# Optimization experiments

Hardware: AMD Instinct MI355X
Metric: run time of the kernel (lower is better)

The kernel has to match this reference:

```python
import jax, jax.numpy as jnp
import numpy as np

NHEAD = 16
EPS = 1e-5


def layer_norm(x, w, b):
    mu = jnp.mean(x, axis=-1, keepdims=True)
    var = jnp.var(x, axis=-1, keepdims=True)
    return (x - mu) * jax.lax.rsqrt(var + EPS) * w + b


def setup_inputs() -> dict:
    key = jax.random.key(0)
    ks = jax.random.split(key, 14)
    B, S, E, F = 16, 1024, 1024, 4096
    s = 0.02
    return {
        "x": jax.random.normal(ks[0], (B, S, E), jnp.float32),
        "in_proj_w": jax.random.normal(ks[1], (3 * E, E), jnp.float32) * s,
        "in_proj_b": jax.random.normal(ks[2], (3 * E,), jnp.float32) * s,
        "out_w": jax.random.normal(ks[3], (E, E), jnp.float32) * s,
        "out_b": jax.random.normal(ks[4], (E,), jnp.float32) * s,
        "lin1_w": jax.random.normal(ks[5], (F, E), jnp.float32) * s,
        "lin1_b": jax.random.normal(ks[6], (F,), jnp.float32) * s,
        "lin2_w": jax.random.normal(ks[7], (E, F), jnp.float32) * s,
        "lin2_b": jax.random.normal(ks[8], (E,), jnp.float32) * s,
        "norm1_w": jnp.ones((E,), jnp.float32),
        "norm1_b": jnp.zeros((E,), jnp.float32),
        "norm2_w": jnp.ones((E,), jnp.float32),
        "norm2_b": jnp.zeros((E,), jnp.float32),
    }


def reference(x, in_proj_w, in_proj_b, out_w, out_b, lin1_w, lin1_b, lin2_w, lin2_b,
              norm1_w, norm1_b, norm2_w, norm2_b):
    B, S, E = x.shape
    H = NHEAD
    D = E // H

    # --- pre-norm self-attention (q = k = v = norm1(x)) ---
    xn = layer_norm(x, norm1_w, norm1_b)
    qkv = xn @ in_proj_w.T + in_proj_b                      # [B,S,3E]
    q, k, v = jnp.split(qkv, 3, axis=-1)
    q = q.reshape(B, S, H, D)
    k = k.reshape(B, S, H, D)
    v = v.reshape(B, S, H, D)
    scale = 1.0 / jnp.sqrt(jnp.asarray(D, x.dtype))
    scores = jnp.einsum("bqhd,bkhd->bhqk", q, k) * scale    # [B,H,S,S]
    attn = jax.nn.softmax(scores, axis=-1)
    ctx = jnp.einsum("bhqk,bkhd->bqhd", attn, v).reshape(B, S, E)
    attn_out = ctx @ out_w.T + out_b
    x = x + attn_out

    # --- pre-norm feedforward (gelu) ---
    xn2 = layer_norm(x, norm2_w, norm2_b)
    h = jax.nn.gelu(xn2 @ lin1_w.T + lin1_b, approximate=False)
    x = x + (h @ lin2_w.T + lin2_b)
    return x
```

## Files before the change

kernel.cpp:

```cpp
#include <hip/hip_runtime.h>


typedef __attribute__((ext_vector_type(8))) short bf16x8;
typedef __attribute__((ext_vector_type(4))) float f32x4;
typedef __attribute__((ext_vector_type(8))) unsigned short u16x8;
typedef __attribute__((ext_vector_type(4))) unsigned short u16x4;

__device__ __forceinline__ float bf2f(unsigned short u) {
    return __uint_as_float(((unsigned int)u) << 16);
}
__device__ __forceinline__ unsigned short f2bf(float f) {
    unsigned int u = __float_as_uint(f);
    u += 0x7fffu + ((u >> 16) & 1u);
    return (unsigned short)(u >> 16);
}
__device__ __forceinline__ unsigned int pkbf_trunc(float a, float b) {
    return (__float_as_uint(a) >> 16) | (__float_as_uint(b) & 0xffff0000u);
}

__device__ __forceinline__ float fast_gelu(float v) {
    const float x = v * 0.70710678118654752f;
    const float ax = fabsf(x);
    const float t = __builtin_amdgcn_rcpf(fmaf(0.3275911f, ax, 1.0f));
    float p = fmaf(1.061405429f, t, -1.453152027f);
    p = fmaf(p, t, 1.421413741f);
    p = fmaf(p, t, -0.284496736f);
    p = fmaf(p, t, 0.254829592f);
    p = p * t;
    const float e = __expf(-x * x);
    float erfv = fmaf(-p, e, 1.0f);
    erfv = (x < 0.0f) ? -erfv : erfv;
    return 0.5f * v * (1.0f + erfv);
}

__device__ __forceinline__ void gload_lds16(const unsigned short* g, unsigned short* l) {
    __builtin_amdgcn_global_load_lds(
        (const __attribute__((address_space(1))) unsigned int*)g,
        (__attribute__((address_space(3))) unsigned int*)l, 16, 0, 0);
}

#define FENCE() asm volatile("" ::: "memory")
#define BAR()                         \
    do {                              \
        FENCE();                      \
        __builtin_amdgcn_s_barrier(); \
        FENCE();                      \
    } while (0)
#define VMCNT(n)                                               \
    do {                                                       \
        asm volatile("s_waitcnt vmcnt(" #n ")" ::: "memory");  \
        __builtin_amdgcn_sched_barrier(0);                     \
    } while (0)

__global__ __launch_bounds__(256) void cvt_kernel(const float* __restrict__ in,
                                                  unsigned short* __restrict__ out, int n4) {
    int i = blockIdx.x * 256 + threadIdx.x;
    if (i >= n4) return;
    float4 v = ((const float4*)in)[i];
    u16x4 o;
    o[0] = f2bf(v.x); o[1] = f2bf(v.y); o[2] = f2bf(v.z); o[3] = f2bf(v.w);
    ((u16x4*)out)[i] = o;
}

__global__ __launch_bounds__(256) void ln_kernel(const float* __restrict__ x,
                                                 const float* __restrict__ w,
                                                 const float* __restrict__ b,
                                                 unsigned short* __restrict__ out) {
    const int row = blockIdx.x;
    const int t = threadIdx.x;
    const float* xr = x + (size_t)row * 1024;
    float4 v = *(const float4*)(xr + t * 4);
    float s = v.x + v.y + v.z + v.w;
    float sq = v.x * v.x + v.y * v.y + v.z * v.z + v.w * v.w;
#pragma unroll
    for (int off = 32; off > 0; off >>= 1) {
        s += __shfl_xor(s, off);
        sq += __shfl_xor(sq, off);
    }
    __shared__ float rs_[4], rq_[4];
    if ((t & 63) == 0) { rs_[t >> 6] = s; rq_[t >> 6] = sq; }
    __syncthreads();
    s = rs_[0] + rs_[1] + rs_[2] + rs_[3];
    sq = rq_[0] + rq_[1] + rq_[2] + rq_[3];
    const float mu = s * (1.0f / 1024.0f);
    const float var = sq * (1.0f / 1024.0f) - mu * mu;
    const float rstd = rsqrtf(var + 1e-5f);
    const int c = t * 4;
    float4 wv = *(const float4*)(w + c);
    float4 bv = *(const float4*)(b + c);
    u16x4 o;
    o[0] = f2bf((v.x - mu) * rstd * wv.x + bv.x);
    o[1] = f2bf((v.y - mu) * rstd * wv.y + bv.y);
    o[2] = f2bf((v.z - mu) * rstd * wv.z + bv.z);
    o[3] = f2bf((v.w - mu) * rstd * wv.w + bv.w);
    *(u16x4*)(out + (size_t)row * 1024 + c) = o;
}

template <int EPI>
__global__ __launch_bounds__(512, 2) void gemm_bt(const unsigned short* __restrict__ A,
                                                  const unsigned short* __restrict__ Bt,
                                                  const float* __restrict__ bias,
                                                  const float* __restrict__ resid,
                                                  void* __restrict__ outp,
                                                  int M, int N, int K, int cnt) {
    __shared__ __align__(16) unsigned short sA[2][256 * 64];
    __shared__ __align__(16) unsigned short sB[2][256 * 64];
    const int t = threadIdx.x;
    const int lane = t & 63;
    const int w = t >> 6;
    const int wm = w >> 2;
    const int wn = w & 3;
    const int quad = lane >> 4;
    const int cl = lane & 15;

    const int GY = M >> 8;
    const int gyl = 31 - __clz(GY);
    const int nt = GY * (N >> 8);
    const int NB = gridDim.x;
    const int g = blockIdx.x;

#define DECODE(gg, mB, nB)                                   \
    do {                                                     \
        const int l_ = ((gg) & 7) * (nt >> 3) + ((gg) >> 3); \
        const int nq_ = l_ >> gyl;                           \
        (nB) = nq_ << 8;                                     \
        (mB) = (l_ - (nq_ << gyl)) << 8;                     \
    } while (0)

    const int swz0 = (quad ^ (cl & 7)) * 16;
    const int swz1 = ((quad + 4) ^ (cl & 7)) * 16;
    const char* aB0 = (const char*)sA + (wm * 128 + cl) * 128 + swz0;
    const char* aB1 = (const char*)sA + (wm * 128 + cl) * 128 + swz1;
    const char* bB0 = (const char*)sB + (wn * 64 + cl) * 128 + swz0;
    const char* bB1 = (const char*)sB + (wn * 64 + cl) * 128 + swz1;

    const int rl = lane >> 3;
    const size_t o8 = (size_t)8 * K;
    const size_t o128 = (size_t)128 * K;
    const size_t thr = (size_t)(w * 16 + rl) * K + (size_t)(((lane & 7) ^ rl) * 8);

#define STG(gp, sbuf, buf, hf, k0)                                                        \
    do {                                                                                  \
        gload_lds16((gp) + (k0) + thr + (hf) * o128,                                      \
                    &sbuf[buf][((hf) * 128 + w * 16) * 64]);                              \
        gload_lds16((gp) + (k0) + thr + (hf) * o128 + o8,                                 \
                    &sbuf[buf][((hf) * 128 + w * 16 + 8) * 64]);                          \
    } while (0)
#define READ_B8(buf)                                                                      \
    do {                                                                                  \
        _Pragma("unroll") for (int nf_ = 0; nf_ < 4; ++nf_) {                             \
            bfr[nf_][0] = *(const bf16x8*)(bB0 + (buf) * 32768 + nf_ * 2048);             \
            bfr[nf_][1] = *(const bf16x8*)(bB1 + (buf) * 32768 + nf_ * 2048);             \
        }                                                                                 \
    } while (0)
#define READ_A2(buf, mfb)                                                                 \
    do {                                                                                  \
        af[0][0] = *(const bf16x8*)(aB0 + (buf) * 32768 + (mfb) * 2048);                  \
        af[0][1] = *(const bf16x8*)(aB1 + (buf) * 32768 + (mfb) * 2048);                  \
        af[1][0] = *(const bf16x8*)(aB0 + (buf) * 32768 + ((mfb) + 1) * 2048);            \
        af[1][1] = *(const bf16x8*)(aB1 + (buf) * 32768 + ((mfb) + 1) * 2048);            \
    } while (0)
#define MFMA_Q(q)                                                                         \
    do {                                                                                  \
        __builtin_amdgcn_s_setprio(1);                                                    \
        _Pragma("unroll") for (int m_ = 0; m_ < 2; ++m_)                                  \
            _Pragma("unroll") for (int nf_ = 0; nf_ < 4; ++nf_)                           \
                _Pragma("unroll") for (int ks_ = 0; ks_ < 2; ++ks_)                       \
                    acc[2 * (q) + m_][nf_] = __builtin_amdgcn_mfma_f32_16x16x32_bf16(     \
                        af[m_][ks_], bfr[nf_][ks_], acc[2 * (q) + m_][nf_], 0, 0, 0);     \
        __builtin_amdgcn_s_setprio(0);                                                    \
    } while (0)

    f32x4 acc[8][4] = {};
    bf16x8 bfr[4][2];
    bf16x8 af[2][2];

    int mBc, nBc, mBn, nBn;
    DECODE(g, mBc, nBc);
    const unsigned short* gAc = A + (size_t)mBc * K;
    const unsigned short* gBc = Bt + (size_t)nBc * K;
    int kc = 0;
    mBn = mBc; nBn = nBc;
    const unsigned short* gAn = gAc;
    const unsigned short* gBn = gBc;
    int kn = 128;
    int tj = 0;

    STG(gAc, sA, 0, 0, kc); STG(gAc, sA, 0, 1, kc);
    STG(gBc, sB, 0, 0, kc); STG(gBc, sB, 0, 1, kc);
    STG(gBc, sB, 1, 0, kc + 64); STG(gBc, sB, 1, 1, kc + 64);
    VMCNT(4);
    BAR();

    const int TP = cnt * (K >> 7);
    for (int P = 0; P < TP; ++P) {
        const bool more = (P + 1 < TP);
        READ_B8(0); READ_A2(0, 0);
        STG(gAc, sA, 1, 0, kc + 64);
        BAR(); MFMA_Q(0); BAR();
        READ_A2(0, 2);
        STG(gAc, sA, 1, 1, kc + 64);
        BAR(); MFMA_Q(1); BAR();
        READ_A2(0, 4);
        if (more) STG(gBn, sB, 0, 0, kn);
        BAR(); MFMA_Q(2); BAR();
        READ_A2(0, 6);
        if (more) STG(gBn, sB, 0, 1, kn);
        BAR(); MFMA_Q(3);
        if (more) { VMCNT(4); } else { VMCNT(0); }
        BAR();
        READ_B8(1); READ_A2(1, 0);
        if (more) STG(gAn, sA, 0, 0, kn);
        BAR(); MFMA_Q(0); BAR();
        READ_A2(1, 2);
        if (more) STG(gAn, sA, 0, 1, kn);
        BAR(); MFMA_Q(1); BAR();
        READ_A2(1, 4);
        if (more) STG(gBn, sB, 1, 0, kn + 64);
        BAR(); MFMA_Q(2); BAR();
        READ_A2(1, 6);
        if (more) STG(gBn, sB, 1, 1, kn + 64);
        BAR(); MFMA_Q(3);
        if (more) VMCNT(4);
        BAR();

        if (kc + 128 == K) {
#pragma unroll
            for (int mf = 0; mf < 8; ++mf) {
                const int rowg = mBc + wm * 128 + mf * 16 + quad * 4;
#pragma unroll
                for (int nf = 0; nf < 4; ++nf) {
                    const int colg = nBc + wn * 64 + nf * 16 + cl;
                    const float bv = bias[colg];
#pragma unroll
                    for (int rr = 0; rr < 4; ++rr) {
                        const float v = acc[mf][nf][rr] + bv;
                        const size_t idx = (size_t)(rowg + rr) * N + colg;
                        if constexpr (EPI == 0) {
                            ((unsigned short*)outp)[idx] = f2bf(v);
                        } else if constexpr (EPI == 1) {
                            ((float*)outp)[idx] = v + resid[idx];
                        } else {
                            ((unsigned short*)outp)[idx] = f2bf(fast_gelu(v));
                        }
                    }
                }
            }
            const f32x4 z = {0.f, 0.f, 0.f, 0.f};
#pragma unroll
            for (int mf = 0; mf < 8; ++mf)
#pragma unroll
                for (int nf = 0; nf < 4; ++nf) acc[mf][nf] = z;
        }
        kc = kn; gAc = gAn; gBc = gBn; mBc = mBn; nBc = nBn;
        kn += 128;
        if (kn >= K) {
            kn = 0;
            ++tj;
            if (tj < cnt) {
                DECODE(g + tj * NB, mBn, nBn);
                gAn = A + (size_t)mBn * K;
                gBn = Bt + (size_t)nBn * K;
            }
        }
    }
#undef STG
#undef READ_B8
#undef READ_A2
#undef MFMA_Q
#undef DECODE
}

__global__ __launch_bounds__(256) void attn_mfma(const unsigned short* __restrict__ qkv,
                                                 unsigned short* __restrict__ ctx) {
    __shared__ __align__(16) unsigned short Ks[64 * 72];
    __shared__ __align__(16) unsigned int Vt[64 * 36];
    __shared__ __align__(16) unsigned short Ps[128 * 72];

    const int bh = blockIdx.x;
    const int qt = blockIdx.y;
    const int b = bh >> 4;
    const int h = bh & 15;
    const int t = threadIdx.x;
    const int w = t >> 6;
    const int lane = t & 63;
    const int quad = lane >> 4;
    const int cl = lane & 15;
    const size_t tok0 = (size_t)b * 1024;
    const int qrow0 = qt * 128 + w * 32;

    bf16x8 aq[2][2];
#pragma unroll
    for (int sub = 0; sub < 2; ++sub) {
        const unsigned short* qp =
            qkv + (tok0 + qrow0 + sub * 16 + cl) * 3072 + h * 64 + quad * 8;
        aq[sub][0] = *(const bf16x8*)(qp);
        aq[sub][1] = *(const bf16x8*)(qp + 32);
    }

    const bf16x8 vones = {0x3F80, 0x3F80, 0x3F80, 0x3F80, 0x3F80, 0x3F80, 0x3F80, 0x3F80};

    const int r0 = t >> 2;
    const int c16 = (t & 3) * 16;
    const int kp = t >> 3;
    const int dc = t & 7;

    f32x4 acc[2][5] = {};
    float m_r[2] = {-3.0e38f, -3.0e38f};

    for (int kt = 0; kt < 16; ++kt) {
        {
            const unsigned short* kg =
                qkv + (tok0 + kt * 64 + r0) * 3072 + 1024 + h * 64 + c16;
            *(int4*)(Ks + r0 * 72 + c16) = *(const int4*)(kg);
            *(int4*)(Ks + r0 * 72 + c16 + 8) = *(const int4*)(kg + 8);

            const unsigned short* vg =
                qkv + (tok0 + kt * 64 + 2 * kp) * 3072 + 2048 + h * 64 + dc * 8;
            u16x8 v0 = *(const u16x8*)(vg);
            u16x8 v1 = *(const u16x8*)(vg + 3072);
            const int g = kp >> 2, wd = kp & 3;
#pragma unroll
            for (int j = 0; j < 8; ++j) {
                const int d = dc * 8 + j;
                Vt[d * 36 + (((g ^ (d >> 3)) << 2) | wd)] =
                    ((unsigned int)v1[j] << 16) | (unsigned int)v0[j];
            }
        }
        __syncthreads();

#pragma unroll
        for (int sub = 0; sub < 2; ++sub) {
            f32x4 sc[4] = {};
#pragma unroll
            for (int i = 0; i < 4; ++i) {
                const int rb = i * 16 + cl;
#pragma unroll
                for (int ks = 0; ks < 2; ++ks) {
                    bf16x8 bk = *(const bf16x8*)(Ks + rb * 72 + quad * 8 + ks * 32);
                    sc[i] = __builtin_amdgcn_mfma_f32_16x16x32_bf16(bk, aq[sub][ks], sc[i],
                                                                    0, 0, 0);
                }
            }
            float mx0 = fmaxf(fmaxf(sc[0][0], sc[0][1]), fmaxf(sc[0][2], sc[0][3]));
            float mx1 = fmaxf(fmaxf(sc[1][0], sc[1][1]), fmaxf(sc[1][2], sc[1][3]));
            float mx2 = fmaxf(fmaxf(sc[2][0], sc[2][1]), fmaxf(sc[2][2], sc[2][3]));
            float mx3 = fmaxf(fmaxf(sc[3][0], sc[3][1]), fmaxf(sc[3][2], sc[3][3]));
            float rmax = fmaxf(fmaxf(mx0, mx1), fmaxf(mx2, mx3));
            rmax = fmaxf(rmax, __shfl_xor(rmax, 16));
            rmax = fmaxf(rmax, __shfl_xor(rmax, 32));
            const float mnew = fmaxf(m_r[sub], rmax * 0.125f);
            const float alpha = __expf(m_r[sub] - mnew);
            m_r[sub] = mnew;
            float al[4];
#pragma unroll
            for (int rr = 0; rr < 4; ++rr) al[rr] = __shfl(alpha, quad * 4 + rr, 16);
#pragma unroll
            for (int j = 0; j < 5; ++j)
#pragma unroll
                for (int rr = 0; rr < 4; ++rr) acc[sub][j][rr] *= al[rr];
            const unsigned short* pr = Ps + (w * 32 + sub * 16 + cl) * 72;
#pragma unroll
            for (int i = 0; i < 4; ++i) {
                const float p0 = __expf(fmaf(sc[i][0], 0.125f, -mnew));
                const float p1 = __expf(fmaf(sc[i][1], 0.125f, -mnew));
                const float p2 = __expf(fmaf(sc[i][2], 0.125f, -mnew));
                const float p3 = __expf(fmaf(sc[i][3], 0.125f, -mnew));
                uint2 pk;
                pk.x = pkbf_trunc(p0, p1);
                pk.y = pkbf_trunc(p2, p3);
                *(uint2*)(pr + i * 16 + quad * 4) = pk;
            }
        }

#pragma unroll
        for (int ks = 0; ks < 2; ++ks) {
            bf16x8 bv[4];
#pragma unroll
            for (int j = 0; j < 4; ++j) {
                const int d = j * 16 + cl;
                bv[j] = *(const bf16x8*)(Vt + d * 36 + (((quad + 4 * ks) ^ (d >> 3)) << 2));
            }
#pragma unroll
            for (int sub = 0; sub < 2; ++sub) {
                bf16x8 ap =
                    *(const bf16x8*)(Ps + (w * 32 + sub * 16 + cl) * 72 + quad * 8 + ks * 32);
#pragma unroll
                for (int j = 0; j < 4; ++j)
                    acc[sub][j] =
                        __builtin_amdgcn_mfma_f32_16x16x32_bf16(ap, bv[j], acc[sub][j], 0, 0, 0);
                acc[sub][4] =
                    __builtin_amdgcn_mfma_f32_16x16x32_bf16(ap, vones, acc[sub][4], 0, 0, 0);
            }
        }
        __syncthreads();
    }

#pragma unroll
    for (int sub = 0; sub < 2; ++sub)
#pragma unroll
        for (int rr = 0; rr < 4; ++rr) {
            const float inv = 1.0f / acc[sub][4][rr];
            const size_t tok = tok0 + qt * 128 + w * 32 + sub * 16 + quad * 4 + rr;
#pragma unroll
            for (int j = 0; j < 4; ++j)
                ctx[tok * 1024 + h * 64 + j * 16 + cl] = f2bf(acc[sub][j][rr] * inv);
        }
}

extern "C" void kernel_launch(void* const* d_in, const int* in_sizes, int n_in,
                              void* d_out, int out_size, void* d_ws, size_t ws_size,
                              hipStream_t stream) {
    const float* x    = (const float*)d_in[0];
    const float* wqkv = (const float*)d_in[1];
    const float* bqkv = (const float*)d_in[2];
    const float* wo   = (const float*)d_in[3];
    const float* bo   = (const float*)d_in[4];
    const float* w1   = (const float*)d_in[5];
    const float* b1   = (const float*)d_in[6];
    const float* w2   = (const float*)d_in[7];
    const float* b2   = (const float*)d_in[8];
    const float* n1w  = (const float*)d_in[9];
    const float* n1b  = (const float*)d_in[10];
    const float* n2w  = (const float*)d_in[11];
    const float* n2b  = (const float*)d_in[12];
    float* out = (float*)d_out;

    char* ws = (char*)d_ws;
    unsigned short* wqkv_b = (unsigned short*)(ws);
    unsigned short* wo_b   = (unsigned short*)(ws + 6291456);
    unsigned short* w1_b   = (unsigned short*)(ws + 8388608);
    unsigned short* w2_b   = (unsigned short*)(ws + 16777216);
    unsigned short* r1     = (unsigned short*)(ws + 25165824);
    unsigned short* r2     = (unsigned short*)(ws + 58720256);

    unsigned short* xn_b  = r1;
    unsigned short* ctx_b = r1;
    unsigned short* xn2_b = r1;
    unsigned short* qkv_b = r2;
    unsigned short* h_b   = r2;

    cvt_kernel<<<3072, 256, 0, stream>>>(wqkv, wqkv_b, 786432);
    cvt_kernel<<<1024, 256, 0, stream>>>(wo, wo_b, 262144);
    cvt_kernel<<<4096, 256, 0, stream>>>(w1, w1_b, 1048576);
    cvt_kernel<<<4096, 256, 0, stream>>>(w2, w2_b, 1048576);

    ln_kernel<<<16384, 256, 0, stream>>>(x, n1w, n1b, xn_b);
    gemm_bt<0><<<256, 512, 0, stream>>>(xn_b, wqkv_b, bqkv, nullptr, qkv_b,
                                        16384, 3072, 1024, 3);
    attn_mfma<<<dim3(256, 8), 256, 0, stream>>>(qkv_b, ctx_b);
    gemm_bt<1><<<256, 512, 0, stream>>>(ctx_b, wo_b, bo, x, out, 16384, 1024, 1024, 1);
    ln_kernel<<<16384, 256, 0, stream>>>(out, n2w, n2b, xn2_b);

    if (ws_size >= 192937984ULL) {
        gemm_bt<2><<<256, 512, 0, stream>>>(xn2_b, w1_b, b1, nullptr, h_b,
                                            16384, 4096, 1024, 4);
        gemm_bt<1><<<256, 512, 0, stream>>>(h_b, w2_b, b2, out, out,
                                            16384, 1024, 4096, 1);
    } else {
        for (int c = 0; c < 2; ++c) {
            const size_t row0 = (size_t)c * 8192;
            gemm_bt<2><<<256, 512, 0, stream>>>(xn2_b + row0 * 1024, w1_b, b1,
                                                nullptr, h_b, 8192, 4096, 1024, 2);
            gemm_bt<1><<<128, 512, 0, stream>>>(h_b, w2_b, b2, out + row0 * 1024,
                                                out + row0 * 1024, 8192, 1024, 4096, 1);
        }
    }
}
```

Baseline: 854.0 us.

## Transpose MFMA operands for vectorized epilogue stores and regroup tile scheduling per XCD

Swaps the A/B operands of the MFMA so each lane's accumulator holds four consecutive columns of one row. The epilogue can then use float4 bias/residual loads and 4-wide bf16 or float4 stores instead of scalar strided ones. It also replaces the tile-index decode with a scheme that gives each group of blocks (by blockIdx mod 8) a contiguous M/N sub-rectangle, aiming for better L2 reuse per XCD. The new NC/MC parameters must match the grid shapes, and a mismatch would leave tiles uncovered.

```diff
diff --git a/kernel.cpp b/kernel.cpp
--- a/kernel.cpp
+++ b/kernel.cpp
@@ -102,7 +102,8 @@
                                                   const float* __restrict__ bias,
                                                   const float* __restrict__ resid,
                                                   void* __restrict__ outp,
-                                                  int M, int N, int K, int cnt) {
+                                                  int M, int N, int K, int cnt,
+                                                  int NC, int MC) {
     __shared__ __align__(16) unsigned short sA[2][256 * 64];
     __shared__ __align__(16) unsigned short sB[2][256 * 64];
     const int t = threadIdx.x;
@@ -113,18 +114,20 @@
     const int quad = lane >> 4;
     const int cl = lane & 15;
 
-    const int GY = M >> 8;
-    const int gyl = 31 - __clz(GY);
-    const int nt = GY * (N >> 8);
     const int NB = gridDim.x;
     const int g = blockIdx.x;
-
-#define DECODE(gg, mB, nB)                                   \
+    const int lpb = NB >> 3;
+    const int xm = (g >> 2) & 1;
+    const int xn = g & 3;
+    const int l0 = g >> 3;
+
+#define DECODE(tjv, mB, nB)                                  \
     do {                                                     \
-        const int l_ = ((gg) & 7) * (nt >> 3) + ((gg) >> 3); \
-        const int nq_ = l_ >> gyl;                           \
-        (nB) = nq_ << 8;                                     \
-        (mB) = (l_ - (nq_ << gyl)) << 8;                     \
+        const int l_ = l0 + (tjv) * lpb;                     \
+        const int mi_ = l_ / NC;                             \
+        const int ni_ = l_ - mi_ * NC;                       \
+        (mB) = (xm * MC + mi_) << 8;                         \
+        (nB) = (xn * NC + ni_) << 8;                         \
     } while (0)
 
     const int swz0 = (quad ^ (cl & 7)) * 16;
@@ -167,7 +170,7 @@
             _Pragma("unroll") for (int nf_ = 0; nf_ < 4; ++nf_)                           \
                 _Pragma("unroll") for (int ks_ = 0; ks_ < 2; ++ks_)                       \
                     acc[2 * (q) + m_][nf_] = __builtin_amdgcn_mfma_f32_16x16x32_bf16(     \
-                        af[m_][ks_], bfr[nf_][ks_], acc[2 * (q) + m_][nf_], 0, 0, 0);     \
+                        bfr[nf_][ks_], af[m_][ks_], acc[2 * (q) + m_][nf_], 0, 0, 0);     \
         __builtin_amdgcn_s_setprio(0);                                                    \
     } while (0)
 
@@ -176,7 +179,7 @@
     bf16x8 af[2][2];
 
     int mBc, nBc, mBn, nBn;
-    DECODE(g, mBc, nBc);
+    DECODE(0, mBc, nBc);
     const unsigned short* gAc = A + (size_t)mBc * K;
     const unsigned short* gBc = Bt + (size_t)nBc * K;
     int kc = 0;
@@ -227,22 +230,32 @@
         if (kc + 128 == K) {
 #pragma unroll
             for (int mf = 0; mf < 8; ++mf) {
-                const int rowg = mBc + wm * 128 + mf * 16 + quad * 4;
+                const int rowg = mBc + wm * 128 + mf * 16 + cl;
+                const size_t rb = (size_t)rowg * N;
 #pragma unroll
                 for (int nf = 0; nf < 4; ++nf) {
-                    const int colg = nBc + wn * 64 + nf * 16 + cl;
-                    const float bv = bias[colg];
-#pragma unroll
-                    for (int rr = 0; rr < 4; ++rr) {
-                        const float v = acc[mf][nf][rr] + bv;
-                        const size_t idx = (size_t)(rowg + rr) * N + colg;
-                        if constexpr (EPI == 0) {
-                            ((unsigned short*)outp)[idx] = f2bf(v);
-                        } else if constexpr (EPI == 1) {
-                            ((float*)outp)[idx] = v + resid[idx];
-                        } else {
-                            ((unsigned short*)outp)[idx] = f2bf(fast_gelu(v));
-                        }
+                    const int colg = nBc + wn * 64 + nf * 16 + quad * 4;
+                    const float4 bv = *(const float4*)(bias + colg);
+                    const f32x4 a = acc[mf][nf];
+                    const size_t idx = rb + colg;
+                    if constexpr (EPI == 0) {
+                        u16x4 o;
+                        o[0] = f2bf(a[0] + bv.x); o[1] = f2bf(a[1] + bv.y);
+                        o[2] = f2bf(a[2] + bv.z); o[3] = f2bf(a[3] + bv.w);
+                        *(u16x4*)((unsigned short*)outp + idx) = o;
+                    } else if constexpr (EPI == 1) {
+                        const float4 rv = *(const float4*)(resid + idx);
+                        float4 o;
+                        o.x = a[0] + bv.x + rv.x; o.y = a[1] + bv.y + rv.y;
+                        o.z = a[2] + bv.z + rv.z; o.w = a[3] + bv.w + rv.w;
+                        *(float4*)((float*)outp + idx) = o;
+                    } else {
+                        u16x4 o;
+                        o[0] = f2bf(fast_gelu(a[0] + bv.x));
+                        o[1] = f2bf(fast_gelu(a[1] + bv.y));
+                        o[2] = f2bf(fast_gelu(a[2] + bv.z));
+                        o[3] = f2bf(fast_gelu(a[3] + bv.w));
+                        *(u16x4*)((unsigned short*)outp + idx) = o;
                     }
                 }
             }
@@ -258,7 +271,7 @@
             kn = 0;
             ++tj;
             if (tj < cnt) {
-                DECODE(g + tj * NB, mBn, nBn);
+                DECODE(tj, mBn, nBn);
                 gAn = A + (size_t)mBn * K;
                 gBn = Bt + (size_t)nBn * K;
             }
@@ -447,23 +460,25 @@
 
     ln_kernel<<<16384, 256, 0, stream>>>(x, n1w, n1b, xn_b);
     gemm_bt<0><<<256, 512, 0, stream>>>(xn_b, wqkv_b, bqkv, nullptr, qkv_b,
-                                        16384, 3072, 1024, 3);
+                                        16384, 3072, 1024, 3, 3, 32);
     attn_mfma<<<dim3(256, 8), 256, 0, stream>>>(qkv_b, ctx_b);
-    gemm_bt<1><<<256, 512, 0, stream>>>(ctx_b, wo_b, bo, x, out, 16384, 1024, 1024, 1);
+    gemm_bt<1><<<256, 512, 0, stream>>>(ctx_b, wo_b, bo, x, out,
+                                        16384, 1024, 1024, 1, 1, 32);
     ln_kernel<<<16384, 256, 0, stream>>>(out, n2w, n2b, xn2_b);
 
     if (ws_size >= 192937984ULL) {
         gemm_bt<2><<<256, 512, 0, stream>>>(xn2_b, w1_b, b1, nullptr, h_b,
-                                            16384, 4096, 1024, 4);
+                                            16384, 4096, 1024, 4, 4, 32);
         gemm_bt<1><<<256, 512, 0, stream>>>(h_b, w2_b, b2, out, out,
-                                            16384, 1024, 4096, 1);
+                                            16384, 1024, 4096, 1, 1, 32);
     } else {
         for (int c = 0; c < 2; ++c) {
             const size_t row0 = (size_t)c * 8192;
             gemm_bt<2><<<256, 512, 0, stream>>>(xn2_b + row0 * 1024, w1_b, b1,
-                                                nullptr, h_b, 8192, 4096, 1024, 2);
+                                                nullptr, h_b, 8192, 4096, 1024, 2, 4, 16);
             gemm_bt<1><<<128, 512, 0, stream>>>(h_b, w2_b, b2, out + row0 * 1024,
-                                                out + row0 * 1024, 8192, 1024, 4096, 1);
+                                                out + row0 * 1024, 8192, 1024, 4096,
+                                                1, 1, 16);
         }
     }
 }
```

Result: slower. 872.7 us (+2.2%).
